# Performance work log

Hardware: AMD Instinct MI355X
Metric: run time of the kernel (lower is better)

The kernel has to match this reference:

```python
import jax, jax.numpy as jnp
import numpy as np

B, N, F, H, HEADS = 2, 256, 64, 64, 4
C = HEADS * H  # n_coefficients (coefficients_mlp is Identity => must equal n_heads*hidden)
EPS = 1e-5
INF = 1e5


def _lin(key, fan_in, fan_out, bias=True):
    k1, k2 = jax.random.split(key)
    w = jax.random.normal(k1, (fan_in, fan_out), jnp.float32) * (1.0 / np.sqrt(fan_in))
    if bias:
        b = jax.random.normal(k2, (fan_out,), jnp.float32) * 0.01
        return w, b
    return w


def setup_inputs() -> dict:
    key = jax.random.key(0)
    ks = jax.random.split(key, 16)
    inp = dict(
        h=jax.random.normal(ks[0], (B, N, F), jnp.float32),
        x=jax.random.normal(ks[1], (B, N, 3), jnp.float32),
        v=jax.random.normal(ks[2], (B, N, 3), jnp.float32),
    )
    inp['edge_w1'], inp['edge_b1'] = _lin(ks[3], 2 * F + 1, H)
    inp['edge_w2'], inp['edge_b2'] = _lin(ks[4], H, H)
    inp['sem_w'], inp['sem_b'] = _lin(ks[5], H, HEADS)
    inp['post_w1'], inp['post_b1'] = _lin(ks[6], C, H)
    inp['post_w2'], inp['post_b2'] = _lin(ks[7], H, H)
    inp['node_w1'], inp['node_b1'] = _lin(ks[8], C + H + F, H)
    inp['node_w2'], inp['node_b2'] = _lin(ks[9], H, F)
    inp['vel_w1'], inp['vel_b1'] = _lin(ks[10], F, H)
    inp['vel_w2'] = _lin(ks[11], H, 1, bias=False) * 0.001  # xavier gain=0.001 analogue
    inp['vmix_w'] = _lin(ks[12], C, 1, bias=False)[:, 0]
    inp['log_gamma'] = -jnp.log(jnp.linspace(1.0, 5.0, HEADS)).astype(jnp.float32)
    return inp


def reference(h, x, v, edge_w1, edge_b1, edge_w2, edge_b2, sem_w, sem_b,
              post_w1, post_b1, post_w2, post_b2, node_w1, node_b1,
              node_w2, node_b2, vel_w1, vel_b1, vel_w2, vmix_w, log_gamma):
    silu = jax.nn.silu
    n = h.shape[-2]
    eye = jnp.eye(n, dtype=h.dtype)[:, :, None]  # [N,N,1] diagonal mask

    # pairwise geometry: entry [i,j] = x_j - x_i
    x_minus_xt = x[..., None, :, :] - x[..., :, None, :]                # [B,N,N,3]
    x_norm = jnp.sqrt((x_minus_xt ** 2).sum(-1, keepdims=True) + EPS)   # [B,N,N,1]

    # pairwise node-feature concat (h_j, h_i) + distance -> edge MLP
    h_j = jnp.broadcast_to(h[..., None, :, :], (B, n, n, F))
    h_i = jnp.broadcast_to(h[..., :, None, :], (B, n, n, F))
    h_cat = jnp.concatenate([h_j, h_i, x_norm], axis=-1)                # [B,N,N,2F+1]
    h_e_mtx = silu(silu(h_cat @ edge_w1 + edge_b1) @ edge_w2 + edge_b2)  # [B,N,N,H]

    # euclidean attention: softmin over j of gamma*dist, diagonal masked out
    dist = (x_norm + INF * eye) * jnp.exp(log_gamma)                    # [B,N,N,heads]
    euclid_att = jax.nn.softmax(-dist, axis=-2)
    # semantic attention: LeakyReLU(0.2) logits, diagonal masked, softmax over j
    sem = jax.nn.leaky_relu(h_e_mtx @ sem_w + sem_b, 0.2) - INF * eye
    sem_att = jax.nn.softmax(sem, axis=-2)
    comb_att = jax.nn.softmax(euclid_att * sem_att, axis=-2)            # [B,N,N,heads]

    # attention-weighted edge features, flattened over (H, heads)
    h_e_att = (h_e_mtx[..., :, None] * comb_att[..., None, :]).reshape(B, n, n, C)

    # spatial attention (coefficients_mlp is Identity)
    unit = x_minus_xt / (x_norm + EPS)                                  # [B,N,N,3]
    # combinations.mean(dim=-3) without materializing [B,N,N,C,3]
    comb_sum = jnp.einsum('bijc,bijd->bicd', h_e_att, unit) / n         # [B,N,C,3]
    comb_norm = (comb_sum ** 2).sum(-1)                                 # [B,N,C]
    h_comb = silu(silu(comb_norm @ post_w1 + post_b1) @ post_w2 + post_b2)

    # delta_v = mean_j (v_mixing over C of combinations)
    delta_v = jnp.einsum('bijc,c,bijd->bid', h_e_att, vmix_w, unit) / n  # [B,N,3]

    h_agg = h_e_att.sum(axis=-2)                                        # sum over j -> [B,N,C]
    out = jnp.concatenate([h, h_agg, h_comb], axis=-1)
    out = silu(silu(out @ node_w1 + node_b1) @ node_w2 + node_b2)
    h_new = h + out                                                     # residual

    # coordinate / velocity update
    v_scale = silu(h_new @ vel_w1 + vel_b1) @ vel_w2                    # [B,N,1]
    v_new = delta_v + v_scale * v
    x_new = x + v_new
    return h_new, x_new, v_new
```

## Files before the change

### kernel.cpp

```cpp
#include <hip/hip_runtime.h>
#include <math.h>

#define EPSV 1e-5f
#define INFV 1e5f

typedef short bf16x8 __attribute__((ext_vector_type(8)));
typedef float f32x4 __attribute__((ext_vector_type(4)));

__device__ __forceinline__ float silu_f(float v) { return v / (1.0f + __expf(-v)); }

__device__ __forceinline__ unsigned short f2bf(float f) {
  unsigned int u = __float_as_uint(f);
  u = (u + 0x7fffu + ((u >> 16) & 1u)) >> 16;
  return (unsigned short)u;
}
__device__ __forceinline__ float bf2f(unsigned short h) {
  return __uint_as_float(((unsigned int)h) << 16);
}

__device__ __forceinline__ float4 br4(float4 v, int op, float4* sc) {
  const int tid = threadIdx.x;
#pragma unroll
  for (int off = 32; off >= 1; off >>= 1) {
    float ox = __shfl_xor(v.x, off);
    float oy = __shfl_xor(v.y, off);
    float oz = __shfl_xor(v.z, off);
    float ow = __shfl_xor(v.w, off);
    if (op) { v.x = fmaxf(v.x, ox); v.y = fmaxf(v.y, oy); v.z = fmaxf(v.z, oz); v.w = fmaxf(v.w, ow); }
    else    { v.x += ox; v.y += oy; v.z += oz; v.w += ow; }
  }
  if ((tid & 63) == 0) sc[tid >> 6] = v;
  __syncthreads();
  float4 r0 = sc[0], r1 = sc[1], r2 = sc[2], r3 = sc[3];
  if (op) {
    v.x = fmaxf(fmaxf(r0.x, r1.x), fmaxf(r2.x, r3.x));
    v.y = fmaxf(fmaxf(r0.y, r1.y), fmaxf(r2.y, r3.y));
    v.z = fmaxf(fmaxf(r0.z, r1.z), fmaxf(r2.z, r3.z));
    v.w = fmaxf(fmaxf(r0.w, r1.w), fmaxf(r2.w, r3.w));
  } else {
    v.x = r0.x + r1.x + r2.x + r3.x;
    v.y = r0.y + r1.y + r2.y + r3.y;
    v.z = r0.z + r1.z + r2.z + r3.z;
    v.w = r0.w + r1.w + r2.w + r3.w;
  }
  __syncthreads();
  return v;
}

__device__ __forceinline__ void gemm64(const unsigned short* TH, const unsigned short* E2T,
                                       int w, int l15, int quad, f32x4 acc[4][4]) {
#pragma unroll
  for (int tr = 0; tr < 4; ++tr)
#pragma unroll
    for (int tc = 0; tc < 4; ++tc)
      acc[tr][tc] = (f32x4){0.f, 0.f, 0.f, 0.f};
#pragma unroll
  for (int ms = 0; ms < 64; ms += 32) {
    bf16x8 af[4], bfr[4];
#pragma unroll
    for (int tr = 0; tr < 4; ++tr)
      af[tr] = *reinterpret_cast<const bf16x8*>(&TH[(64 * w + 16 * tr + l15) * 72 + ms + quad * 8]);
#pragma unroll
    for (int tc = 0; tc < 4; ++tc)
      bfr[tc] = *reinterpret_cast<const bf16x8*>(&E2T[(16 * tc + l15) * 72 + ms + quad * 8]);
#pragma unroll
    for (int tr = 0; tr < 4; ++tr)
#pragma unroll
      for (int tc = 0; tc < 4; ++tc)
        acc[tr][tc] = __builtin_amdgcn_mfma_f32_16x16x32_bf16(af[tr], bfr[tc], acc[tr][tc], 0, 0, 0);
  }
}

__global__ __launch_bounds__(256) void k_all(
    const float* __restrict__ h, const float* __restrict__ x, const float* __restrict__ v,
    const float* __restrict__ ew1, const float* __restrict__ eb1,
    const float* __restrict__ ew2, const float* __restrict__ eb2,
    const float* __restrict__ semw, const float* __restrict__ semb,
    const float* __restrict__ pw1, const float* __restrict__ pb1,
    const float* __restrict__ pw2, const float* __restrict__ pb2,
    const float* __restrict__ nw1, const float* __restrict__ nb1,
    const float* __restrict__ nw2, const float* __restrict__ nb2,
    const float* __restrict__ vw1, const float* __restrict__ vb1,
    const float* __restrict__ vw2, const float* __restrict__ vmix,
    const float* __restrict__ lgam, float* __restrict__ out) {

  __shared__ __align__(16) unsigned short TH[256 * 72];
  __shared__ __align__(16) char E2u[9216];
  __shared__ __align__(16) float4 unit_l[256];
  __shared__ __align__(16) float4 cat_l[256];
  __shared__ float dn_l[256];
  __shared__ float addk[64];
  __shared__ float w1dk[64];

  unsigned short* E2T = (unsigned short*)E2u;
  float4* sc    = (float4*)E2u;
  float*  dvs   = (float*)(E2u + 128);
  float*  cn_l  = (float*)(E2u + 256);
  float*  hag_l = (float*)(E2u + 1280);
  float*  tmp   = (float*)(E2u + 2304);
  float*  m1s   = (float*)(E2u + 3328);
  float*  hnw   = (float*)(E2u + 3584);
  float*  nin   = (float*)(E2u + 4096);

  const int bi  = blockIdx.x;
  const int i   = bi & 255;
  const int b0  = bi & ~255;
  const int tid = threadIdx.x;
  const int j   = tid;
  const int bj  = b0 | j;

  const float xi0 = x[bi * 3 + 0], xi1 = x[bi * 3 + 1], xi2 = x[bi * 3 + 2];
  const float dx = x[bj * 3 + 0] - xi0;
  const float dy = x[bj * 3 + 1] - xi1;
  const float dz = x[bj * 3 + 2] - xi2;
  const float dn = sqrtf(dx * dx + dy * dy + dz * dz + EPSV);
  const float invn = 1.0f / (dn + EPSV);
  const float ux = dx * invn, uy = dy * invn, uz = dz * invn;
  unit_l[j] = make_float4(ux, uy, uz, 0.f);
  dn_l[j] = dn;

  {
    const float4* hb4 = reinterpret_cast<const float4*>(h + (size_t)b0 * 64);
#pragma unroll
    for (int q = 0; q < 16; ++q) {
      int idx = q * 256 + tid;
      float4 f4 = hb4[idx];
      int row = idx >> 4, c4 = idx & 15;
      uint2 pk;
      pk.x = (unsigned int)f2bf(f4.x) | ((unsigned int)f2bf(f4.y) << 16);
      pk.y = (unsigned int)f2bf(f4.z) | ((unsigned int)f2bf(f4.w) << 16);
      *reinterpret_cast<uint2*>(&TH[row * 72 + c4 * 4]) = pk;
    }
  }
#pragma unroll
  for (int q = 0; q < 16; ++q) {
    int idx = q * 256 + tid;
    E2T[(idx & 63) * 72 + (idx >> 6)] = f2bf(ew1[idx]);
  }
  {
    int s = tid >> 6, k = tid & 63;
    const float* hrow = h + (size_t)bi * 64;
    float bp = 0.f;
#pragma unroll
    for (int f2 = 0; f2 < 16; ++f2) {
      int f = s * 16 + f2;
      bp += hrow[f] * ew1[(64 + f) * 64 + k];
    }
    reinterpret_cast<float*>(cat_l)[s * 64 + k] = bp;
  }
  __syncthreads();
  if (tid < 64) {
    const float* catf = reinterpret_cast<float*>(cat_l);
    addk[tid] = eb1[tid] + catf[tid] + catf[64 + tid] + catf[128 + tid] + catf[192 + tid];
    w1dk[tid] = ew1[128 * 64 + tid];
  }

  const int lid  = tid & 63;
  const int w    = tid >> 6;
  const int l15  = lid & 15;
  const int quad = lid >> 4;

  f32x4 acc[4][4];
  gemm64(TH, E2T, w, l15, quad, acc);
  __syncthreads();

#pragma unroll
  for (int tc = 0; tc < 4; ++tc) {
    float ak = addk[16 * tc + l15];
    float wd = w1dk[16 * tc + l15];
#pragma unroll
    for (int tr = 0; tr < 4; ++tr)
#pragma unroll
      for (int r = 0; r < 4; ++r) {
        int row = 64 * w + 16 * tr + quad * 4 + r;
        float val = silu_f(acc[tr][tc][r] + ak + dn_l[row] * wd);
        TH[row * 72 + 16 * tc + l15] = f2bf(val);
      }
  }
#pragma unroll
  for (int q = 0; q < 16; ++q) {
    int idx = q * 256 + tid;
    E2T[(idx & 63) * 72 + (idx >> 6)] = f2bf(ew2[idx]);
  }
  __syncthreads();

  gemm64(TH, E2T, w, l15, quad, acc);
  __syncthreads();

#pragma unroll
  for (int tc = 0; tc < 4; ++tc) {
    float b2 = eb2[16 * tc + l15];
#pragma unroll
    for (int tr = 0; tr < 4; ++tr)
#pragma unroll
      for (int r = 0; r < 4; ++r) {
        int row = 64 * w + 16 * tr + quad * 4 + r;
        TH[row * 68 + 16 * tc + l15] = f2bf(silu_f(acc[tr][tc][r] + b2));
      }
  }
  __syncthreads();

  float he[64];
#pragma unroll
  for (int c = 0; c < 16; ++c) {
    uint2 u = *reinterpret_cast<const uint2*>(&TH[tid * 68 + c * 4]);
    he[c * 4 + 0] = __uint_as_float(u.x << 16);
    he[c * 4 + 1] = __uint_as_float(u.x & 0xffff0000u);
    he[c * 4 + 2] = __uint_as_float(u.y << 16);
    he[c * 4 + 3] = __uint_as_float(u.y & 0xffff0000u);
  }

  float4 sl = *reinterpret_cast<const float4*>(semb);
#pragma unroll
  for (int k = 0; k < 64; ++k) {
    float4 sw = *reinterpret_cast<const float4*>(semw + k * 4);
    sl.x += he[k] * sw.x; sl.y += he[k] * sw.y;
    sl.z += he[k] * sw.z; sl.w += he[k] * sw.w;
  }
  const float diag = (j == i) ? INFV : 0.0f;
  sl.x = ((sl.x > 0.f) ? sl.x : 0.2f * sl.x) - diag;
  sl.y = ((sl.y > 0.f) ? sl.y : 0.2f * sl.y) - diag;
  sl.z = ((sl.z > 0.f) ? sl.z : 0.2f * sl.z) - diag;
  sl.w = ((sl.w > 0.f) ? sl.w : 0.2f * sl.w) - diag;

  float4 lg = *reinterpret_cast<const float4*>(lgam);
  const float dni = dn + diag;
  float4 e_eu = make_float4(__expf(-dni * __expf(lg.x)), __expf(-dni * __expf(lg.y)),
                            __expf(-dni * __expf(lg.z)), __expf(-dni * __expf(lg.w)));

  float4 M = br4(sl, 1, sc);
  float4 e_sem = make_float4(__expf(sl.x - M.x), __expf(sl.y - M.y),
                             __expf(sl.z - M.z), __expf(sl.w - M.w));

  float4 a8 = e_eu, b8 = e_sem;
#pragma unroll
  for (int off = 32; off >= 1; off >>= 1) {
    a8.x += __shfl_xor(a8.x, off); a8.y += __shfl_xor(a8.y, off);
    a8.z += __shfl_xor(a8.z, off); a8.w += __shfl_xor(a8.w, off);
    b8.x += __shfl_xor(b8.x, off); b8.y += __shfl_xor(b8.y, off);
    b8.z += __shfl_xor(b8.z, off); b8.w += __shfl_xor(b8.w, off);
  }
  if ((tid & 63) == 0) { sc[tid >> 6] = a8; sc[4 + (tid >> 6)] = b8; }
  __syncthreads();
  float4 Se, Ss;
  {
    float4 r0 = sc[0], r1 = sc[1], r2 = sc[2], r3 = sc[3];
    Se = make_float4(r0.x + r1.x + r2.x + r3.x, r0.y + r1.y + r2.y + r3.y,
                     r0.z + r1.z + r2.z + r3.z, r0.w + r1.w + r2.w + r3.w);
    float4 s0 = sc[4], s1 = sc[5], s2 = sc[6], s3 = sc[7];
    Ss = make_float4(s0.x + s1.x + s2.x + s3.x, s0.y + s1.y + s2.y + s3.y,
                     s0.z + s1.z + s2.z + s3.z, s0.w + s1.w + s2.w + s3.w);
  }
  __syncthreads();

  float4 p = make_float4((e_eu.x / Se.x) * (e_sem.x / Ss.x), (e_eu.y / Se.y) * (e_sem.y / Ss.y),
                         (e_eu.z / Se.z) * (e_sem.z / Ss.z), (e_eu.w / Se.w) * (e_sem.w / Ss.w));
  float4 ep = make_float4(__expf(p.x), __expf(p.y), __expf(p.z), __expf(p.w));
  float4 Sp = br4(ep, 0, sc);
  float4 catt = make_float4(ep.x / Sp.x, ep.y / Sp.y, ep.z / Sp.z, ep.w / Sp.w);
  cat_l[j] = catt;

  float s = 0.f;
#pragma unroll
  for (int k = 0; k < 64; ++k) {
    float4 vm = *reinterpret_cast<const float4*>(vmix + k * 4);
    s += he[k] * (catt.x * vm.x + catt.y * vm.y + catt.z * vm.z + catt.w * vm.w);
  }
  float4 dv = br4(make_float4(s * ux, s * uy, s * uz, 0.f), 0, sc);
  if (j == 0) {
    const float inv = 1.0f / 256.0f;
    dvs[0] = dv.x * inv; dvs[1] = dv.y * inv; dvs[2] = dv.z * inv;
  }

  {
    const int kk = lid & 15;
    const int jq = lid >> 4;
    const int k  = 16 * w + kk;
    float agg[4] = {0.f, 0.f, 0.f, 0.f};
    float ax[4]  = {0.f, 0.f, 0.f, 0.f};
    float ay[4]  = {0.f, 0.f, 0.f, 0.f};
    float az[4]  = {0.f, 0.f, 0.f, 0.f};
#pragma unroll 4
    for (int jr2 = 0; jr2 < 64; ++jr2) {
      int jj = jq * 64 + ((jr2 + 4 * jq) & 63);
      float hev = bf2f(TH[jj * 68 + k]);
      float4 ca = cat_l[jj];
      float4 u  = unit_l[jj];
      float w0 = hev * ca.x, w1 = hev * ca.y, w2 = hev * ca.z, w3 = hev * ca.w;
      agg[0] += w0; agg[1] += w1; agg[2] += w2; agg[3] += w3;
      ax[0] += w0 * u.x; ay[0] += w0 * u.y; az[0] += w0 * u.z;
      ax[1] += w1 * u.x; ay[1] += w1 * u.y; az[1] += w1 * u.z;
      ax[2] += w2 * u.x; ay[2] += w2 * u.y; az[2] += w2 * u.z;
      ax[3] += w3 * u.x; ay[3] += w3 * u.y; az[3] += w3 * u.z;
    }
#pragma unroll
    for (int off = 16; off <= 32; off <<= 1) {
#pragma unroll
      for (int hd = 0; hd < 4; ++hd) {
        agg[hd] += __shfl_xor(agg[hd], off);
        ax[hd]  += __shfl_xor(ax[hd], off);
        ay[hd]  += __shfl_xor(ay[hd], off);
        az[hd]  += __shfl_xor(az[hd], off);
      }
    }
    if (jq == 0) {
      const float inv = 1.0f / 256.0f;
#pragma unroll
      for (int hd = 0; hd < 4; ++hd) {
        float cx = ax[hd] * inv, cy = ay[hd] * inv, cz = az[hd] * inv;
        cn_l[k * 4 + hd]  = cx * cx + cy * cy + cz * cz;
        hag_l[k * 4 + hd] = agg[hd];
      }
    }
  }
  __syncthreads();

  const int k = tid & 63;
  {
    float a = 0.f;
    for (int m2 = 0; m2 < 64; ++m2) {
      int m = w * 64 + m2;
      a += cn_l[m] * pw1[m * 64 + k];
    }
    tmp[tid] = a;
  }
  __syncthreads();
  if (tid < 64) m1s[tid] = silu_f(pb1[tid] + tmp[tid] + tmp[64 + tid] + tmp[128 + tid] + tmp[192 + tid]);
  __syncthreads();
  {
    float a = 0.f;
#pragma unroll
    for (int m2 = 0; m2 < 16; ++m2) {
      int m = w * 16 + m2;
      a += m1s[m] * pw2[m * 64 + k];
    }
    tmp[tid] = a;
  }
  nin[64 + tid] = hag_l[tid];
  __syncthreads();
  if (tid < 64) {
    nin[tid] = h[(size_t)bi * 64 + tid];
    nin[320 + tid] = silu_f(pb2[tid] + tmp[tid] + tmp[64 + tid] + tmp[128 + tid] + tmp[192 + tid]);
  }
  __syncthreads();
  {
    float a = 0.f;
    for (int m2 = 0; m2 < 96; ++m2) {
      int m = w * 96 + m2;
      a += nin[m] * nw1[m * 64 + k];
    }
    tmp[tid] = a;
  }
  __syncthreads();
  if (tid < 64) m1s[tid] = silu_f(nb1[tid] + tmp[tid] + tmp[64 + tid] + tmp[128 + tid] + tmp[192 + tid]);
  __syncthreads();
  {
    float a = 0.f;
#pragma unroll
    for (int m2 = 0; m2 < 16; ++m2) {
      int m = w * 16 + m2;
      a += m1s[m] * nw2[m * 64 + k];
    }
    tmp[tid] = a;
  }
  __syncthreads();
  if (tid < 64) {
    float hn = h[(size_t)bi * 64 + tid] +
               silu_f(nb2[tid] + tmp[tid] + tmp[64 + tid] + tmp[128 + tid] + tmp[192 + tid]);
    out[(size_t)bi * 64 + tid] = hn;
    hnw[tid] = hn;
  }
  __syncthreads();
  {
    float a = 0.f;
#pragma unroll
    for (int m2 = 0; m2 < 16; ++m2) {
      int m = w * 16 + m2;
      a += hnw[m] * vw1[m * 64 + k];
    }
    tmp[tid] = a;
  }
  __syncthreads();
  if (tid < 64) {
    float vh = silu_f(vb1[tid] + tmp[tid] + tmp[64 + tid] + tmp[128 + tid] + tmp[192 + tid]) * vw2[tid];
#pragma unroll
    for (int off = 32; off >= 1; off >>= 1) vh += __shfl_xor(vh, off);
    if (tid == 0) {
#pragma unroll
      for (int d = 0; d < 3; ++d) {
        float vn = dvs[d] + vh * v[bi * 3 + d];
        out[32768 + bi * 3 + d] = x[bi * 3 + d] + vn;
        out[34304 + bi * 3 + d] = vn;
      }
    }
  }
}

extern "C" void kernel_launch(void* const* d_in, const int* in_sizes, int n_in,
                              void* d_out, int out_size, void* d_ws, size_t ws_size,
                              hipStream_t stream) {
  const float* h    = (const float*)d_in[0];
  const float* x    = (const float*)d_in[1];
  const float* v    = (const float*)d_in[2];
  const float* ew1  = (const float*)d_in[3];
  const float* eb1  = (const float*)d_in[4];
  const float* ew2  = (const float*)d_in[5];
  const float* eb2  = (const float*)d_in[6];
  const float* semw = (const float*)d_in[7];
  const float* semb = (const float*)d_in[8];
  const float* pw1  = (const float*)d_in[9];
  const float* pb1  = (const float*)d_in[10];
  const float* pw2  = (const float*)d_in[11];
  const float* pb2  = (const float*)d_in[12];
  const float* nw1  = (const float*)d_in[13];
  const float* nb1  = (const float*)d_in[14];
  const float* nw2  = (const float*)d_in[15];
  const float* nb2  = (const float*)d_in[16];
  const float* vw1  = (const float*)d_in[17];
  const float* vb1  = (const float*)d_in[18];
  const float* vw2  = (const float*)d_in[19];
  const float* vmix = (const float*)d_in[20];
  const float* lgam = (const float*)d_in[21];
  float* out = (float*)d_out;

  k_all<<<512, 256, 0, stream>>>(h, x, v, ew1, eb1, ew2, eb2, semw, semb,
                                 pw1, pb1, pw2, pb2, nw1, nb1, nw2, nb2,
                                 vw1, vb1, vw2, vmix, lgam, out);
}
```

Before: 141.9 us.

## Split node-update tail into separate kernel and compute semantic logits via MFMA

The fused kernel is split in two. A pair kernel writes the per-node coefficient norms, aggregates and delta_v to workspace. A small 64-thread tail kernel then runs the post, node and velocity MLPs, replacing the 256-thread block's chain of syncs and partial sums. The per-pair semantic-attention and v-mixing dot products become a bf16 MFMA against a packed weight tile, instead of scalar FMAs over register copies of the edge features. Divisions become hardware reciprocals, bf16 packing uses the packed intrinsic, and the edge-feature LDS stride changes to 72. The trade-offs are an extra launch, a workspace round trip, and slightly lower precision in the logits and reciprocals.

```diff
diff --git a/kernel.cpp b/kernel.cpp
--- a/kernel.cpp
+++ b/kernel.cpp
@@ -1,4 +1,5 @@
 #include <hip/hip_runtime.h>
+#include <hip/hip_bf16.h>
 #include <math.h>
 
 #define EPSV 1e-5f
@@ -7,7 +8,8 @@
 typedef short bf16x8 __attribute__((ext_vector_type(8)));
 typedef float f32x4 __attribute__((ext_vector_type(4)));
 
-__device__ __forceinline__ float silu_f(float v) { return v / (1.0f + __expf(-v)); }
+__device__ __forceinline__ float rcp_f(float x) { return __builtin_amdgcn_rcpf(x); }
+__device__ __forceinline__ float silu_f(float v) { return v * rcp_f(1.0f + __expf(-v)); }
 
 __device__ __forceinline__ unsigned short f2bf(float f) {
   unsigned int u = __float_as_uint(f);
@@ -16,6 +18,13 @@
 }
 __device__ __forceinline__ float bf2f(unsigned short h) {
   return __uint_as_float(((unsigned int)h) << 16);
+}
+__device__ __forceinline__ unsigned int pkbf(float a, float b) {
+  float2 f2; f2.x = a; f2.y = b;
+  __hip_bfloat162 t = __float22bfloat162_rn(f2);
+  unsigned int u;
+  __builtin_memcpy(&u, &t, 4);
+  return u;
 }
 
 __device__ __forceinline__ float4 br4(float4 v, int op, float4* sc) {
@@ -71,36 +80,23 @@
   }
 }
 
-__global__ __launch_bounds__(256) void k_all(
-    const float* __restrict__ h, const float* __restrict__ x, const float* __restrict__ v,
+__global__ __launch_bounds__(256) void k_pair(
+    const float* __restrict__ h, const float* __restrict__ x,
     const float* __restrict__ ew1, const float* __restrict__ eb1,
     const float* __restrict__ ew2, const float* __restrict__ eb2,
     const float* __restrict__ semw, const float* __restrict__ semb,
-    const float* __restrict__ pw1, const float* __restrict__ pb1,
-    const float* __restrict__ pw2, const float* __restrict__ pb2,
-    const float* __restrict__ nw1, const float* __restrict__ nb1,
-    const float* __restrict__ nw2, const float* __restrict__ nb2,
-    const float* __restrict__ vw1, const float* __restrict__ vb1,
-    const float* __restrict__ vw2, const float* __restrict__ vmix,
-    const float* __restrict__ lgam, float* __restrict__ out) {
+    const float* __restrict__ vmix, const float* __restrict__ lgam,
+    float* __restrict__ CN, float* __restrict__ HAG, float* __restrict__ DVW) {
 
   __shared__ __align__(16) unsigned short TH[256 * 72];
-  __shared__ __align__(16) char E2u[9216];
+  __shared__ __align__(16) unsigned short E2T[64 * 72];
+  __shared__ __align__(16) float sd[256 * 8];
   __shared__ __align__(16) float4 unit_l[256];
   __shared__ __align__(16) float4 cat_l[256];
   __shared__ float dn_l[256];
   __shared__ float addk[64];
   __shared__ float w1dk[64];
-
-  unsigned short* E2T = (unsigned short*)E2u;
-  float4* sc    = (float4*)E2u;
-  float*  dvs   = (float*)(E2u + 128);
-  float*  cn_l  = (float*)(E2u + 256);
-  float*  hag_l = (float*)(E2u + 1280);
-  float*  tmp   = (float*)(E2u + 2304);
-  float*  m1s   = (float*)(E2u + 3328);
-  float*  hnw   = (float*)(E2u + 3584);
-  float*  nin   = (float*)(E2u + 4096);
+  __shared__ float4 sc[8];
 
   const int bi  = blockIdx.x;
   const int i   = bi & 255;
@@ -114,7 +110,7 @@
   const float dy = x[bj * 3 + 1] - xi1;
   const float dz = x[bj * 3 + 2] - xi2;
   const float dn = sqrtf(dx * dx + dy * dy + dz * dz + EPSV);
-  const float invn = 1.0f / (dn + EPSV);
+  const float invn = rcp_f(dn + EPSV);
   const float ux = dx * invn, uy = dy * invn, uz = dz * invn;
   unit_l[j] = make_float4(ux, uy, uz, 0.f);
   dn_l[j] = dn;
@@ -127,8 +123,8 @@
       float4 f4 = hb4[idx];
       int row = idx >> 4, c4 = idx & 15;
       uint2 pk;
-      pk.x = (unsigned int)f2bf(f4.x) | ((unsigned int)f2bf(f4.y) << 16);
-      pk.y = (unsigned int)f2bf(f4.z) | ((unsigned int)f2bf(f4.w) << 16);
+      pk.x = pkbf(f4.x, f4.y);
+      pk.y = pkbf(f4.z, f4.w);
       *reinterpret_cast<uint2*>(&TH[row * 72 + c4 * 4]) = pk;
     }
   }
@@ -195,29 +191,47 @@
 #pragma unroll
       for (int r = 0; r < 4; ++r) {
         int row = 64 * w + 16 * tr + quad * 4 + r;
-        TH[row * 68 + 16 * tc + l15] = f2bf(silu_f(acc[tr][tc][r] + b2));
+        TH[row * 72 + 16 * tc + l15] = f2bf(silu_f(acc[tr][tc][r] + b2));
       }
   }
-  __syncthreads();
-
-  float he[64];
-#pragma unroll
-  for (int c = 0; c < 16; ++c) {
-    uint2 u = *reinterpret_cast<const uint2*>(&TH[tid * 68 + c * 4]);
-    he[c * 4 + 0] = __uint_as_float(u.x << 16);
-    he[c * 4 + 1] = __uint_as_float(u.x & 0xffff0000u);
-    he[c * 4 + 2] = __uint_as_float(u.y << 16);
-    he[c * 4 + 3] = __uint_as_float(u.y & 0xffff0000u);
-  }
-
-  float4 sl = *reinterpret_cast<const float4*>(semb);
-#pragma unroll
-  for (int k = 0; k < 64; ++k) {
-    float4 sw = *reinterpret_cast<const float4*>(semw + k * 4);
-    sl.x += he[k] * sw.x; sl.y += he[k] * sw.y;
-    sl.z += he[k] * sw.z; sl.w += he[k] * sw.w;
-  }
+#pragma unroll
+  for (int q = 0; q < 2; ++q) {
+    int idx = q * 256 + tid;
+    int n = idx >> 6, kk = idx & 63;
+    float wv = (n < 4) ? semw[kk * 4 + n] : vmix[kk * 4 + (n - 4)];
+    E2T[n * 72 + kk] = f2bf(wv);
+  }
+  __syncthreads();
+
+  {
+    f32x4 acc3[4];
+#pragma unroll
+    for (int tr = 0; tr < 4; ++tr) acc3[tr] = (f32x4){0.f, 0.f, 0.f, 0.f};
+#pragma unroll
+    for (int ms = 0; ms < 64; ms += 32) {
+      bf16x8 b3 = *reinterpret_cast<const bf16x8*>(&E2T[l15 * 72 + ms + quad * 8]);
+#pragma unroll
+      for (int tr = 0; tr < 4; ++tr) {
+        bf16x8 a3 = *reinterpret_cast<const bf16x8*>(&TH[(64 * w + 16 * tr + l15) * 72 + ms + quad * 8]);
+        acc3[tr] = __builtin_amdgcn_mfma_f32_16x16x32_bf16(a3, b3, acc3[tr], 0, 0, 0);
+      }
+    }
+    if (l15 < 8) {
+#pragma unroll
+      for (int tr = 0; tr < 4; ++tr)
+#pragma unroll
+        for (int r = 0; r < 4; ++r)
+          sd[(64 * w + 16 * tr + quad * 4 + r) * 8 + l15] = acc3[tr][r];
+    }
+  }
+  __syncthreads();
+
+  float4 s01 = *reinterpret_cast<const float4*>(sd + j * 8);
+  float4 s23 = *reinterpret_cast<const float4*>(sd + j * 8 + 4);
+  float4 sbv = *reinterpret_cast<const float4*>(semb);
   const float diag = (j == i) ? INFV : 0.0f;
+  float4 sl;
+  sl.x = s01.x + sbv.x; sl.y = s01.y + sbv.y; sl.z = s01.z + sbv.z; sl.w = s01.w + sbv.w;
   sl.x = ((sl.x > 0.f) ? sl.x : 0.2f * sl.x) - diag;
   sl.y = ((sl.y > 0.f) ? sl.y : 0.2f * sl.y) - diag;
   sl.z = ((sl.z > 0.f) ? sl.z : 0.2f * sl.z) - diag;
@@ -253,23 +267,23 @@
   }
   __syncthreads();
 
-  float4 p = make_float4((e_eu.x / Se.x) * (e_sem.x / Ss.x), (e_eu.y / Se.y) * (e_sem.y / Ss.y),
-                         (e_eu.z / Se.z) * (e_sem.z / Ss.z), (e_eu.w / Se.w) * (e_sem.w / Ss.w));
+  float4 p = make_float4((e_eu.x * rcp_f(Se.x)) * (e_sem.x * rcp_f(Ss.x)),
+                         (e_eu.y * rcp_f(Se.y)) * (e_sem.y * rcp_f(Ss.y)),
+                         (e_eu.z * rcp_f(Se.z)) * (e_sem.z * rcp_f(Ss.z)),
+                         (e_eu.w * rcp_f(Se.w)) * (e_sem.w * rcp_f(Ss.w)));
   float4 ep = make_float4(__expf(p.x), __expf(p.y), __expf(p.z), __expf(p.w));
   float4 Sp = br4(ep, 0, sc);
-  float4 catt = make_float4(ep.x / Sp.x, ep.y / Sp.y, ep.z / Sp.z, ep.w / Sp.w);
+  float4 catt = make_float4(ep.x * rcp_f(Sp.x), ep.y * rcp_f(Sp.y),
+                            ep.z * rcp_f(Sp.z), ep.w * rcp_f(Sp.w));
   cat_l[j] = catt;
 
-  float s = 0.f;
-#pragma unroll
-  for (int k = 0; k < 64; ++k) {
-    float4 vm = *reinterpret_cast<const float4*>(vmix + k * 4);
-    s += he[k] * (catt.x * vm.x + catt.y * vm.y + catt.z * vm.z + catt.w * vm.w);
-  }
+  float s = catt.x * s23.x + catt.y * s23.y + catt.z * s23.z + catt.w * s23.w;
   float4 dv = br4(make_float4(s * ux, s * uy, s * uz, 0.f), 0, sc);
   if (j == 0) {
     const float inv = 1.0f / 256.0f;
-    dvs[0] = dv.x * inv; dvs[1] = dv.y * inv; dvs[2] = dv.z * inv;
+    DVW[bi * 3 + 0] = dv.x * inv;
+    DVW[bi * 3 + 1] = dv.y * inv;
+    DVW[bi * 3 + 2] = dv.z * inv;
   }
 
   {
@@ -283,7 +297,7 @@
 #pragma unroll 4
     for (int jr2 = 0; jr2 < 64; ++jr2) {
       int jj = jq * 64 + ((jr2 + 4 * jq) & 63);
-      float hev = bf2f(TH[jj * 68 + k]);
+      float hev = bf2f(TH[jj * 72 + k]);
       float4 ca = cat_l[jj];
       float4 u  = unit_l[jj];
       float w0 = hev * ca.x, w1 = hev * ca.y, w2 = hev * ca.z, w3 = hev * ca.w;
@@ -305,93 +319,80 @@
     }
     if (jq == 0) {
       const float inv = 1.0f / 256.0f;
+      f32x4 cnv, hgv;
 #pragma unroll
       for (int hd = 0; hd < 4; ++hd) {
         float cx = ax[hd] * inv, cy = ay[hd] * inv, cz = az[hd] * inv;
-        cn_l[k * 4 + hd]  = cx * cx + cy * cy + cz * cz;
-        hag_l[k * 4 + hd] = agg[hd];
+        cnv[hd] = cx * cx + cy * cy + cz * cz;
+        hgv[hd] = agg[hd];
       }
-    }
-  }
-  __syncthreads();
-
-  const int k = tid & 63;
-  {
-    float a = 0.f;
-    for (int m2 = 0; m2 < 64; ++m2) {
-      int m = w * 64 + m2;
-      a += cn_l[m] * pw1[m * 64 + k];
-    }
-    tmp[tid] = a;
-  }
-  __syncthreads();
-  if (tid < 64) m1s[tid] = silu_f(pb1[tid] + tmp[tid] + tmp[64 + tid] + tmp[128 + tid] + tmp[192 + tid]);
-  __syncthreads();
-  {
-    float a = 0.f;
-#pragma unroll
-    for (int m2 = 0; m2 < 16; ++m2) {
-      int m = w * 16 + m2;
-      a += m1s[m] * pw2[m * 64 + k];
-    }
-    tmp[tid] = a;
-  }
-  nin[64 + tid] = hag_l[tid];
-  __syncthreads();
-  if (tid < 64) {
-    nin[tid] = h[(size_t)bi * 64 + tid];
-    nin[320 + tid] = silu_f(pb2[tid] + tmp[tid] + tmp[64 + tid] + tmp[128 + tid] + tmp[192 + tid]);
-  }
-  __syncthreads();
-  {
-    float a = 0.f;
-    for (int m2 = 0; m2 < 96; ++m2) {
-      int m = w * 96 + m2;
-      a += nin[m] * nw1[m * 64 + k];
-    }
-    tmp[tid] = a;
-  }
-  __syncthreads();
-  if (tid < 64) m1s[tid] = silu_f(nb1[tid] + tmp[tid] + tmp[64 + tid] + tmp[128 + tid] + tmp[192 + tid]);
-  __syncthreads();
-  {
-    float a = 0.f;
-#pragma unroll
-    for (int m2 = 0; m2 < 16; ++m2) {
-      int m = w * 16 + m2;
-      a += m1s[m] * nw2[m * 64 + k];
-    }
-    tmp[tid] = a;
-  }
-  __syncthreads();
-  if (tid < 64) {
-    float hn = h[(size_t)bi * 64 + tid] +
-               silu_f(nb2[tid] + tmp[tid] + tmp[64 + tid] + tmp[128 + tid] + tmp[192 + tid]);
-    out[(size_t)bi * 64 + tid] = hn;
-    hnw[tid] = hn;
-  }
-  __syncthreads();
-  {
-    float a = 0.f;
-#pragma unroll
-    for (int m2 = 0; m2 < 16; ++m2) {
-      int m = w * 16 + m2;
-      a += hnw[m] * vw1[m * 64 + k];
-    }
-    tmp[tid] = a;
-  }
-  __syncthreads();
-  if (tid < 64) {
-    float vh = silu_f(vb1[tid] + tmp[tid] + tmp[64 + tid] + tmp[128 + tid] + tmp[192 + tid]) * vw2[tid];
-#pragma unroll
-    for (int off = 32; off >= 1; off >>= 1) vh += __shfl_xor(vh, off);
-    if (tid == 0) {
-#pragma unroll
-      for (int d = 0; d < 3; ++d) {
-        float vn = dvs[d] + vh * v[bi * 3 + d];
-        out[32768 + bi * 3 + d] = x[bi * 3 + d] + vn;
-        out[34304 + bi * 3 + d] = vn;
-      }
+      *reinterpret_cast<f32x4*>(CN  + (size_t)bi * 256 + k * 4) = cnv;
+      *reinterpret_cast<f32x4*>(HAG + (size_t)bi * 256 + k * 4) = hgv;
+    }
+  }
+}
+
+__global__ __launch_bounds__(64) void k_tail(
+    const float* __restrict__ h, const float* __restrict__ x, const float* __restrict__ v,
+    const float* __restrict__ pw1, const float* __restrict__ pb1,
+    const float* __restrict__ pw2, const float* __restrict__ pb2,
+    const float* __restrict__ nw1, const float* __restrict__ nb1,
+    const float* __restrict__ nw2, const float* __restrict__ nb2,
+    const float* __restrict__ vw1, const float* __restrict__ vb1,
+    const float* __restrict__ vw2,
+    const float* __restrict__ CN, const float* __restrict__ HAG,
+    const float* __restrict__ DVW, float* __restrict__ out) {
+  __shared__ __align__(16) float cn_s[256];
+  __shared__ __align__(16) float hag_s[256];
+  __shared__ float h_s[64];
+  __shared__ float m1[64];
+  __shared__ float hc[64];
+  __shared__ float hn_s[64];
+
+  const int bi = blockIdx.x;
+  const int k  = threadIdx.x;
+
+  reinterpret_cast<float4*>(cn_s)[k]  = reinterpret_cast<const float4*>(CN  + (size_t)bi * 256)[k];
+  reinterpret_cast<float4*>(hag_s)[k] = reinterpret_cast<const float4*>(HAG + (size_t)bi * 256)[k];
+  h_s[k] = h[(size_t)bi * 64 + k];
+  __syncthreads();
+
+  float a = pb1[k];
+  for (int m = 0; m < 256; ++m) a += cn_s[m] * pw1[m * 64 + k];
+  m1[k] = silu_f(a);
+  __syncthreads();
+  a = pb2[k];
+#pragma unroll 8
+  for (int m = 0; m < 64; ++m) a += m1[m] * pw2[m * 64 + k];
+  hc[k] = silu_f(a);
+  __syncthreads();
+  a = nb1[k];
+#pragma unroll 4
+  for (int m = 0; m < 64; ++m)  a += h_s[m] * nw1[m * 64 + k];
+  for (int m = 0; m < 256; ++m) a += hag_s[m] * nw1[(64 + m) * 64 + k];
+#pragma unroll 4
+  for (int m = 0; m < 64; ++m)  a += hc[m] * nw1[(320 + m) * 64 + k];
+  m1[k] = silu_f(a);
+  __syncthreads();
+  a = nb2[k];
+#pragma unroll 8
+  for (int m = 0; m < 64; ++m) a += m1[m] * nw2[m * 64 + k];
+  float hn = h_s[k] + silu_f(a);
+  out[(size_t)bi * 64 + k] = hn;
+  hn_s[k] = hn;
+  __syncthreads();
+  a = vb1[k];
+#pragma unroll 8
+  for (int m = 0; m < 64; ++m) a += hn_s[m] * vw1[m * 64 + k];
+  float vh = silu_f(a) * vw2[k];
+#pragma unroll
+  for (int off = 32; off >= 1; off >>= 1) vh += __shfl_xor(vh, off);
+  if (k == 0) {
+#pragma unroll
+    for (int d = 0; d < 3; ++d) {
+      float vn = DVW[bi * 3 + d] + vh * v[bi * 3 + d];
+      out[32768 + bi * 3 + d] = x[bi * 3 + d] + vn;
+      out[34304 + bi * 3 + d] = vn;
     }
   }
 }
@@ -423,7 +424,13 @@
   const float* lgam = (const float*)d_in[21];
   float* out = (float*)d_out;
 
-  k_all<<<512, 256, 0, stream>>>(h, x, v, ew1, eb1, ew2, eb2, semw, semb,
-                                 pw1, pb1, pw2, pb2, nw1, nb1, nw2, nb2,
-                                 vw1, vb1, vw2, vmix, lgam, out);
-}
+  float* ws  = (float*)d_ws;
+  float* CN  = ws;
+  float* HAG = ws + 131072;
+  float* DVW = ws + 262144;
+
+  k_pair<<<512, 256, 0, stream>>>(h, x, ew1, eb1, ew2, eb2, semw, semb,
+                                  vmix, lgam, CN, HAG, DVW);
+  k_tail<<<512, 64, 0, stream>>>(h, x, v, pw1, pb1, pw2, pb2, nw1, nb1, nw2, nb2,
+                                 vw1, vb1, vw2, CN, HAG, DVW, out);
+}
```

New measurement: 141.6 us. No clear change (-0.2%).

## Move semantic and vmix projections to MFMA, shrink LDS and registers for occupancy

Applied to the files above, without the earlier changes.

Each thread's 64-float he[] register array and its scalar dot products with sem_w and vmix_w are replaced by a small bf16 MFMA GEMM. That GEMM computes 8 outputs per edge, which are staged in shared memory. Shared memory is reorganised by aliasing cat_l, tmp, nin and related buffers onto the TH and E2 scratch, and dn is packed into unit_l.w. Launch bounds now request 3 blocks per CU. Divisions become hardware rcp, and bf16 packing uses a packed intrinsic. The aliasing requires extra __syncthreads calls, and the attention logits and vmix now run at bf16 weight precision.

```diff
diff --git a/kernel.cpp b/kernel.cpp
--- a/kernel.cpp
+++ b/kernel.cpp
@@ -1,4 +1,5 @@
 #include <hip/hip_runtime.h>
+#include <hip/hip_bf16.h>
 #include <math.h>
 
 #define EPSV 1e-5f
@@ -7,7 +8,8 @@
 typedef short bf16x8 __attribute__((ext_vector_type(8)));
 typedef float f32x4 __attribute__((ext_vector_type(4)));
 
-__device__ __forceinline__ float silu_f(float v) { return v / (1.0f + __expf(-v)); }
+__device__ __forceinline__ float rcp_f(float x) { return __builtin_amdgcn_rcpf(x); }
+__device__ __forceinline__ float silu_f(float v) { return v * rcp_f(1.0f + __expf(-v)); }
 
 __device__ __forceinline__ unsigned short f2bf(float f) {
   unsigned int u = __float_as_uint(f);
@@ -16,6 +18,13 @@
 }
 __device__ __forceinline__ float bf2f(unsigned short h) {
   return __uint_as_float(((unsigned int)h) << 16);
+}
+__device__ __forceinline__ unsigned int pkbf(float a, float b) {
+  float2 f2; f2.x = a; f2.y = b;
+  __hip_bfloat162 t = __float22bfloat162_rn(f2);
+  unsigned int u;
+  __builtin_memcpy(&u, &t, 4);
+  return u;
 }
 
 __device__ __forceinline__ float4 br4(float4 v, int op, float4* sc) {
@@ -71,7 +80,7 @@
   }
 }
 
-__global__ __launch_bounds__(256) void k_all(
+__global__ __launch_bounds__(256, 3) void k_all(
     const float* __restrict__ h, const float* __restrict__ x, const float* __restrict__ v,
     const float* __restrict__ ew1, const float* __restrict__ eb1,
     const float* __restrict__ ew2, const float* __restrict__ eb2,
@@ -87,20 +96,21 @@
   __shared__ __align__(16) unsigned short TH[256 * 72];
   __shared__ __align__(16) char E2u[9216];
   __shared__ __align__(16) float4 unit_l[256];
-  __shared__ __align__(16) float4 cat_l[256];
-  __shared__ float dn_l[256];
   __shared__ float addk[64];
   __shared__ float w1dk[64];
+  __shared__ __align__(16) float bms[256];
 
   unsigned short* E2T = (unsigned short*)E2u;
-  float4* sc    = (float4*)E2u;
-  float*  dvs   = (float*)(E2u + 128);
-  float*  cn_l  = (float*)(E2u + 256);
-  float*  hag_l = (float*)(E2u + 1280);
-  float*  tmp   = (float*)(E2u + 2304);
-  float*  m1s   = (float*)(E2u + 3328);
-  float*  hnw   = (float*)(E2u + 3584);
-  float*  nin   = (float*)(E2u + 4096);
+  float*  sd    = (float*)E2u;
+  float4* cat_l = (float4*)E2u;
+  float*  cn_l  = (float*)(E2u + 4096);
+  float*  hag_l = (float*)(E2u + 5120);
+  float4* sc    = (float4*)(E2u + 8192);
+  float*  dvs   = (float*)(E2u + 8320);
+  float* tmp = (float*)TH;
+  float* m1s = (float*)TH + 256;
+  float* hnw = (float*)TH + 320;
+  float* nin = (float*)TH + 384;
 
   const int bi  = blockIdx.x;
   const int i   = bi & 255;
@@ -114,10 +124,9 @@
   const float dy = x[bj * 3 + 1] - xi1;
   const float dz = x[bj * 3 + 2] - xi2;
   const float dn = sqrtf(dx * dx + dy * dy + dz * dz + EPSV);
-  const float invn = 1.0f / (dn + EPSV);
+  const float invn = rcp_f(dn + EPSV);
   const float ux = dx * invn, uy = dy * invn, uz = dz * invn;
-  unit_l[j] = make_float4(ux, uy, uz, 0.f);
-  dn_l[j] = dn;
+  unit_l[j] = make_float4(ux, uy, uz, dn);
 
   {
     const float4* hb4 = reinterpret_cast<const float4*>(h + (size_t)b0 * 64);
@@ -127,8 +136,8 @@
       float4 f4 = hb4[idx];
       int row = idx >> 4, c4 = idx & 15;
       uint2 pk;
-      pk.x = (unsigned int)f2bf(f4.x) | ((unsigned int)f2bf(f4.y) << 16);
-      pk.y = (unsigned int)f2bf(f4.z) | ((unsigned int)f2bf(f4.w) << 16);
+      pk.x = pkbf(f4.x, f4.y);
+      pk.y = pkbf(f4.z, f4.w);
       *reinterpret_cast<uint2*>(&TH[row * 72 + c4 * 4]) = pk;
     }
   }
@@ -146,12 +155,11 @@
       int f = s * 16 + f2;
       bp += hrow[f] * ew1[(64 + f) * 64 + k];
     }
-    reinterpret_cast<float*>(cat_l)[s * 64 + k] = bp;
+    bms[s * 64 + k] = bp;
   }
   __syncthreads();
   if (tid < 64) {
-    const float* catf = reinterpret_cast<float*>(cat_l);
-    addk[tid] = eb1[tid] + catf[tid] + catf[64 + tid] + catf[128 + tid] + catf[192 + tid];
+    addk[tid] = eb1[tid] + bms[tid] + bms[64 + tid] + bms[128 + tid] + bms[192 + tid];
     w1dk[tid] = ew1[128 * 64 + tid];
   }
 
@@ -173,7 +181,7 @@
 #pragma unroll
       for (int r = 0; r < 4; ++r) {
         int row = 64 * w + 16 * tr + quad * 4 + r;
-        float val = silu_f(acc[tr][tc][r] + ak + dn_l[row] * wd);
+        float val = silu_f(acc[tr][tc][r] + ak + unit_l[row].w * wd);
         TH[row * 72 + 16 * tc + l15] = f2bf(val);
       }
   }
@@ -195,29 +203,48 @@
 #pragma unroll
       for (int r = 0; r < 4; ++r) {
         int row = 64 * w + 16 * tr + quad * 4 + r;
-        TH[row * 68 + 16 * tc + l15] = f2bf(silu_f(acc[tr][tc][r] + b2));
-      }
-  }
-  __syncthreads();
-
-  float he[64];
-#pragma unroll
-  for (int c = 0; c < 16; ++c) {
-    uint2 u = *reinterpret_cast<const uint2*>(&TH[tid * 68 + c * 4]);
-    he[c * 4 + 0] = __uint_as_float(u.x << 16);
-    he[c * 4 + 1] = __uint_as_float(u.x & 0xffff0000u);
-    he[c * 4 + 2] = __uint_as_float(u.y << 16);
-    he[c * 4 + 3] = __uint_as_float(u.y & 0xffff0000u);
-  }
-
-  float4 sl = *reinterpret_cast<const float4*>(semb);
-#pragma unroll
-  for (int k = 0; k < 64; ++k) {
-    float4 sw = *reinterpret_cast<const float4*>(semw + k * 4);
-    sl.x += he[k] * sw.x; sl.y += he[k] * sw.y;
-    sl.z += he[k] * sw.z; sl.w += he[k] * sw.w;
-  }
+        TH[row * 72 + 16 * tc + l15] = f2bf(silu_f(acc[tr][tc][r] + b2));
+      }
+  }
+#pragma unroll
+  for (int q = 0; q < 2; ++q) {
+    int idx = q * 256 + tid;
+    int n = idx >> 6, kk = idx & 63;
+    float wv = (n < 4) ? semw[kk * 4 + n] : vmix[kk * 4 + (n - 4)];
+    E2T[n * 72 + kk] = f2bf(wv);
+  }
+  __syncthreads();
+
+  f32x4 acc3[4];
+  {
+#pragma unroll
+    for (int tr = 0; tr < 4; ++tr) acc3[tr] = (f32x4){0.f, 0.f, 0.f, 0.f};
+#pragma unroll
+    for (int ms = 0; ms < 64; ms += 32) {
+      bf16x8 b3 = *reinterpret_cast<const bf16x8*>(&E2T[l15 * 72 + ms + quad * 8]);
+#pragma unroll
+      for (int tr = 0; tr < 4; ++tr) {
+        bf16x8 a3 = *reinterpret_cast<const bf16x8*>(&TH[(64 * w + 16 * tr + l15) * 72 + ms + quad * 8]);
+        acc3[tr] = __builtin_amdgcn_mfma_f32_16x16x32_bf16(a3, b3, acc3[tr], 0, 0, 0);
+      }
+    }
+  }
+  __syncthreads();
+  if (l15 < 8) {
+#pragma unroll
+    for (int tr = 0; tr < 4; ++tr)
+#pragma unroll
+      for (int r = 0; r < 4; ++r)
+        sd[(64 * w + 16 * tr + quad * 4 + r) * 8 + l15] = acc3[tr][r];
+  }
+  __syncthreads();
+
+  float4 s01 = *reinterpret_cast<const float4*>(sd + j * 8);
+  float4 s23 = *reinterpret_cast<const float4*>(sd + j * 8 + 4);
+  float4 sbv = *reinterpret_cast<const float4*>(semb);
   const float diag = (j == i) ? INFV : 0.0f;
+  float4 sl;
+  sl.x = s01.x + sbv.x; sl.y = s01.y + sbv.y; sl.z = s01.z + sbv.z; sl.w = s01.w + sbv.w;
   sl.x = ((sl.x > 0.f) ? sl.x : 0.2f * sl.x) - diag;
   sl.y = ((sl.y > 0.f) ? sl.y : 0.2f * sl.y) - diag;
   sl.z = ((sl.z > 0.f) ? sl.z : 0.2f * sl.z) - diag;
@@ -253,19 +280,17 @@
   }
   __syncthreads();
 
-  float4 p = make_float4((e_eu.x / Se.x) * (e_sem.x / Ss.x), (e_eu.y / Se.y) * (e_sem.y / Ss.y),
-                         (e_eu.z / Se.z) * (e_sem.z / Ss.z), (e_eu.w / Se.w) * (e_sem.w / Ss.w));
+  float4 p = make_float4((e_eu.x * rcp_f(Se.x)) * (e_sem.x * rcp_f(Ss.x)),
+                         (e_eu.y * rcp_f(Se.y)) * (e_sem.y * rcp_f(Ss.y)),
+                         (e_eu.z * rcp_f(Se.z)) * (e_sem.z * rcp_f(Ss.z)),
+                         (e_eu.w * rcp_f(Se.w)) * (e_sem.w * rcp_f(Ss.w)));
   float4 ep = make_float4(__expf(p.x), __expf(p.y), __expf(p.z), __expf(p.w));
   float4 Sp = br4(ep, 0, sc);
-  float4 catt = make_float4(ep.x / Sp.x, ep.y / Sp.y, ep.z / Sp.z, ep.w / Sp.w);
+  float4 catt = make_float4(ep.x * rcp_f(Sp.x), ep.y * rcp_f(Sp.y),
+                            ep.z * rcp_f(Sp.z), ep.w * rcp_f(Sp.w));
   cat_l[j] = catt;
 
-  float s = 0.f;
-#pragma unroll
-  for (int k = 0; k < 64; ++k) {
-    float4 vm = *reinterpret_cast<const float4*>(vmix + k * 4);
-    s += he[k] * (catt.x * vm.x + catt.y * vm.y + catt.z * vm.z + catt.w * vm.w);
-  }
+  float s = catt.x * s23.x + catt.y * s23.y + catt.z * s23.z + catt.w * s23.w;
   float4 dv = br4(make_float4(s * ux, s * uy, s * uz, 0.f), 0, sc);
   if (j == 0) {
     const float inv = 1.0f / 256.0f;
@@ -283,7 +308,7 @@
 #pragma unroll 4
     for (int jr2 = 0; jr2 < 64; ++jr2) {
       int jj = jq * 64 + ((jr2 + 4 * jq) & 63);
-      float hev = bf2f(TH[jj * 68 + k]);
+      float hev = bf2f(TH[jj * 72 + k]);
       float4 ca = cat_l[jj];
       float4 u  = unit_l[jj];
       float w0 = hev * ca.x, w1 = hev * ca.y, w2 = hev * ca.z, w3 = hev * ca.w;
@@ -334,9 +359,11 @@
       int m = w * 16 + m2;
       a += m1s[m] * pw2[m * 64 + k];
     }
+    float hgv = hag_l[tid];
+    __syncthreads();
     tmp[tid] = a;
-  }
-  nin[64 + tid] = hag_l[tid];
+    nin[64 + tid] = hgv;
+  }
   __syncthreads();
   if (tid < 64) {
     nin[tid] = h[(size_t)bi * 64 + tid];
@@ -349,6 +376,7 @@
       int m = w * 96 + m2;
       a += nin[m] * nw1[m * 64 + k];
     }
+    __syncthreads();
     tmp[tid] = a;
   }
   __syncthreads();
@@ -361,6 +389,7 @@
       int m = w * 16 + m2;
       a += m1s[m] * nw2[m * 64 + k];
     }
+    __syncthreads();
     tmp[tid] = a;
   }
   __syncthreads();
@@ -378,6 +407,7 @@
       int m = w * 16 + m2;
       a += hnw[m] * vw1[m * 64 + k];
     }
+    __syncthreads();
     tmp[tid] = a;
   }
   __syncthreads();
```

Result: faster. 121.9 us (-14.1%).
